# Optimization experiments

Hardware: AMD Instinct MI355X
Metric: run time of the kernel (lower is better)

Reference implementation:

```python
import jax, jax.numpy as jnp
import numpy as np

N_NODES = 100000
N_EDGES = 3200000
N_GRAPHS = 64
DIMS = [512, 1024, 512, 256, 128, 64, 32]
N_CLASSES = 10


def setup_inputs() -> dict:
    key = jax.random.key(0)
    ks = jax.random.split(key, 20)
    inp = {}
    inp['h'] = jax.random.normal(ks[0], (N_NODES, DIMS[0]), dtype=jnp.float32)
    inp['src'] = jax.random.randint(ks[1], (N_EDGES,), 0, N_NODES, dtype=jnp.int32)
    inp['dst'] = jax.random.randint(ks[2], (N_EDGES,), 0, N_NODES, dtype=jnp.int32)
    inp['graph_ids'] = jnp.sort(jax.random.randint(ks[3], (N_NODES,), 0, N_GRAPHS, dtype=jnp.int32))
    # GraphConv weights (glorot-like) and biases for the 6 layers
    for i in range(6):
        fi, fo = DIMS[i], DIMS[i + 1]
        scale = jnp.sqrt(2.0 / (fi + fo)).astype(jnp.float32)
        inp[f'W{i+1}'] = jax.random.normal(ks[4 + i], (fi, fo), dtype=jnp.float32) * scale
        inp[f'b{i+1}'] = jnp.zeros((fo,), dtype=jnp.float32)
    inp['Wc'] = jax.random.normal(ks[12], (DIMS[-1], N_CLASSES), dtype=jnp.float32) * 0.1
    inp['bc'] = jnp.zeros((N_CLASSES,), dtype=jnp.float32)
    return inp


def _graph_conv(h, W, b, src, dst, out_inv_sqrt, in_inv_sqrt):
    """DGL GraphConv, norm='both': D_dst^{-1/2} A (D_src^{-1/2} h) W + b.
    Apply W first when it shrinks the feature dim (DGL's mult-first trick)."""
    fi, fo = W.shape
    if fi > fo:
        h = h @ W  # shrink before aggregating
    h = h * out_inv_sqrt[:, None]
    agg = jax.ops.segment_sum(h[src], dst, num_segments=N_NODES)  # SpMM
    agg = agg * in_inv_sqrt[:, None]
    if fi <= fo:
        agg = agg @ W
    return agg + b


def reference(h, src, dst, graph_ids, W1, b1, W2, b2, W3, b3, W4, b4, W5, b5, W6, b6, Wc, bc):
    ones_e = jnp.ones((N_EDGES,), dtype=jnp.float32)
    out_deg = jax.ops.segment_sum(ones_e, src, num_segments=N_NODES)
    in_deg = jax.ops.segment_sum(ones_e, dst, num_segments=N_NODES)
    out_inv_sqrt = jax.lax.rsqrt(jnp.clip(out_deg, 1.0))  # allow_zero_in_degree -> clamp
    in_inv_sqrt = jax.lax.rsqrt(jnp.clip(in_deg, 1.0))
    for (W, b) in [(W1, b1), (W2, b2), (W3, b3), (W4, b4), (W5, b5), (W6, b6)]:
        h = jax.nn.relu(_graph_conv(h, W, b, src, dst, out_inv_sqrt, in_inv_sqrt))
    # dgl.mean_nodes over batched graph
    sums = jax.ops.segment_sum(h, graph_ids, num_segments=N_GRAPHS)
    counts = jax.ops.segment_sum(jnp.ones((N_NODES,), jnp.float32), graph_ids, num_segments=N_GRAPHS)
    hg = sums / jnp.clip(counts, 1.0)[:, None]
    return hg @ Wc + bc  # [N_GRAPHS, n_classes]
```

## Files before the change

### kernel.cpp

```cpp
#include <hip/hip_runtime.h>

#define N_NODES 100000
#define N_EDGES 3200000
#define N_GRAPHS 64
#define M_PAD   100096
#define CAP     128

typedef unsigned short u16;
typedef __bf16 bf16x8 __attribute__((ext_vector_type(8)));
typedef float f32x4 __attribute__((ext_vector_type(4)));
typedef unsigned int u32x4 __attribute__((ext_vector_type(4)));
typedef __attribute__((address_space(3))) unsigned int lds_u32;
typedef __attribute__((address_space(1))) unsigned int glb_u32;

__device__ inline u16 f2bf(float f) {
  unsigned u = __float_as_uint(f);
  unsigned r = (u + 0x7fffu + ((u >> 16) & 1u)) >> 16;
  return (u16)r;
}
__device__ inline float bf2f(u16 h) {
  return __uint_as_float(((unsigned)h) << 16);
}

#define E4 (N_EDGES / 4)
__global__ void k_build(const int* __restrict__ src, const int* __restrict__ dst,
                        int* __restrict__ odeg, int* __restrict__ cur,
                        int* __restrict__ colp) {
  int t = blockIdx.x * blockDim.x + threadIdx.x;
  if (t >= E4) return;
  int s[4], d[4], pos[4];
  #pragma unroll
  for (int q = 0; q < 4; ++q) {
    int e = t + q * E4;
    s[q] = src[e];
    d[q] = dst[e];
  }
  #pragma unroll
  for (int q = 0; q < 4; ++q) atomicAdd(&odeg[s[q]], 1);
  #pragma unroll
  for (int q = 0; q < 4; ++q) pos[q] = atomicAdd(&cur[d[q]], 1);
  #pragma unroll
  for (int q = 0; q < 4; ++q)
    if (pos[q] < CAP)
      __builtin_nontemporal_store(s[q], &colp[(size_t)d[q] * CAP + pos[q]]);
}

__global__ void k_rsqrt(const int* __restrict__ odeg, const int* __restrict__ ideg,
                        float* __restrict__ a, float* __restrict__ bI) {
  int v = blockIdx.x * blockDim.x + threadIdx.x;
  if (v < N_NODES) {
    a[v]  = rsqrtf(fmaxf((float)odeg[v], 1.0f));
    bI[v] = rsqrtf(fmaxf((float)ideg[v], 1.0f));
  }
}

__global__ void k_prep(const float* __restrict__ x, const float* __restrict__ ascl,
                       u16* __restrict__ y) {
  int i = blockIdx.x * blockDim.x + threadIdx.x;
  if (i >= N_NODES * 128) return;
  int row = i >> 7;
  float s = ascl[row];
  float4 v = ((const float4*)x)[i];
  uint2 o;
  o.x = (unsigned)f2bf(v.x * s) | ((unsigned)f2bf(v.y * s) << 16);
  o.y = (unsigned)f2bf(v.z * s) | ((unsigned)f2bf(v.w * s) << 16);
  ((uint2*)y)[i] = o;
}

__global__ void k_wt(const float* __restrict__ W, u16* __restrict__ Wt, int fi, int fo) {
  int idx = blockIdx.x * blockDim.x + threadIdx.x;
  if (idx >= fi * fo) return;
  int n = idx / fi, k = idx % fi;
  Wt[idx] = f2bf(W[(size_t)k * fo + n]);
}

template<int BM, int BN, int WM, int WN>
__global__ __launch_bounds__(256) void k_mfma(
    const u16* __restrict__ A, const u16* __restrict__ Wt,
    const float* __restrict__ bias, const float* __restrict__ rowscale,
    u16* __restrict__ C, int N, int K, int flags)
{
  constexpr int BK = 32;
  constexpr int WX = BN / WN;
  constexpr int WY = BM / WM;
  static_assert(WX * WY == 4, "4 waves");
  constexpr int TM = WM / 16;
  constexpr int TN = WN / 16;
  constexpr int CA = BM / 16;
  constexpr int CB = BN / 16;

  __shared__ __align__(1024) u16 As[BM * BK];
  __shared__ __align__(1024) u16 Bs[BN * BK];

  const int G   = gridDim.x;
  const int lin = blockIdx.x;
  const int xcd = lin & 7, pp = lin >> 3;
  const int q8  = G >> 3,  r8 = G & 7;
  const int nbid = (xcd < r8 ? xcd * (q8 + 1) : r8 * (q8 + 1) + (xcd - r8) * q8) + pp;
  const int gx = N / BN;
  const int bm = (nbid / gx) * BM;
  const int bn = (nbid % gx) * BN;

  const int tid  = threadIdx.x;
  const int wave = tid >> 6;
  const int lane = tid & 63;
  const int wx = wave % WX;
  const int wy = wave / WX;

  const int lm = lane & 15;
  const int lc = lane >> 4;

  const int srA = (lane >> 2);
  const int spA = lane & 3;
  f32x4 acc[TM][TN] = {};

  for (int k0 = 0; k0 < K; k0 += BK) {
    #pragma unroll
    for (int q0 = 0; q0 < CA; q0 += 4) {
      int q = q0 + wave;
      if (q < CA) {
        int rl = q * 16 + srA;
        int c  = (spA - (rl >> 1)) & 3;
        const u16* g = A + (size_t)(bm + rl) * K + k0 + c * 8;
        __builtin_amdgcn_global_load_lds((const glb_u32*)g, (lds_u32*)(As + q * 512), 16, 0, 0);
      }
    }
    #pragma unroll
    for (int q0 = 0; q0 < CB; q0 += 4) {
      int q = q0 + wave;
      if (q < CB) {
        int rl = q * 16 + srA;
        int c  = (spA - (rl >> 1)) & 3;
        const u16* g = Wt + (size_t)(bn + rl) * K + k0 + c * 8;
        __builtin_amdgcn_global_load_lds((const glb_u32*)g, (lds_u32*)(Bs + q * 512), 16, 0, 0);
      }
    }
    __syncthreads();

    bf16x8 af[TM], bfr[TN];
    #pragma unroll
    for (int i = 0; i < TM; ++i) {
      int rl = wy * WM + i * 16 + lm;
      int p = (lc + (rl >> 1)) & 3;
      af[i] = *(const bf16x8*)(As + rl * 32 + p * 8);
    }
    #pragma unroll
    for (int j = 0; j < TN; ++j) {
      int rl = wx * WN + j * 16 + lm;
      int p = (lc + (rl >> 1)) & 3;
      bfr[j] = *(const bf16x8*)(Bs + rl * 32 + p * 8);
    }
    #pragma unroll
    for (int i = 0; i < TM; ++i)
      #pragma unroll
      for (int j = 0; j < TN; ++j)
        acc[i][j] = __builtin_amdgcn_mfma_f32_16x16x32_bf16(af[i], bfr[j], acc[i][j], 0, 0, 0);
    __syncthreads();
  }

  const bool do_br = flags & 1;
  const bool do_rs = flags & 2;
  #pragma unroll
  for (int i = 0; i < TM; ++i) {
    #pragma unroll
    for (int j = 0; j < TN; ++j) {
      int col = bn + wx * WN + j * 16 + lm;
      float bv = do_br ? bias[col] : 0.f;
      #pragma unroll
      for (int r = 0; r < 4; ++r) {
        int row = bm + wy * WM + i * 16 + lc * 4 + r;
        float v = acc[i][j][r];
        if (do_rs) v *= rowscale[row];
        if (do_br) v = fmaxf(v + bv, 0.f);
        C[(size_t)row * N + col] = f2bf(v);
      }
    }
  }
}

template<int D>
__global__ __launch_bounds__(256) void k_spmm(
    const int* __restrict__ deg, const int* __restrict__ colp,
    const u16* __restrict__ X, const float* __restrict__ dscale,
    const float* __restrict__ bias, u16* __restrict__ Y, int relu_bias)
{
  constexpr int TPR = D / 8;
  constexpr int EPW = 64 / TPR;
  const int lane = threadIdx.x & 63;
  const int node = blockIdx.x * 4 + (threadIdx.x >> 6);
  const int g = lane / TPR;
  const int c = (lane % TPR) * 8;
  const int* cl = colp + (size_t)node * CAP;
  int e = deg[node];
  e = e < CAP ? e : CAP;
  float acc[8] = {};
  int j = 0;
  for (; j + 4 * EPW <= e; j += 4 * EPW) {
    int u0 = cl[j + g];
    int u1 = cl[j + g + EPW];
    int u2 = cl[j + g + 2 * EPW];
    int u3 = cl[j + g + 3 * EPW];
    u32x4 v0 = *(const u32x4*)(X + (size_t)u0 * D + c);
    u32x4 v1 = *(const u32x4*)(X + (size_t)u1 * D + c);
    u32x4 v2 = *(const u32x4*)(X + (size_t)u2 * D + c);
    u32x4 v3 = *(const u32x4*)(X + (size_t)u3 * D + c);
    #pragma unroll
    for (int q = 0; q < 4; ++q) {
      acc[2*q]   += __uint_as_float(v0[q] << 16);
      acc[2*q+1] += __uint_as_float(v0[q] & 0xffff0000u);
      acc[2*q]   += __uint_as_float(v1[q] << 16);
      acc[2*q+1] += __uint_as_float(v1[q] & 0xffff0000u);
      acc[2*q]   += __uint_as_float(v2[q] << 16);
      acc[2*q+1] += __uint_as_float(v2[q] & 0xffff0000u);
      acc[2*q]   += __uint_as_float(v3[q] << 16);
      acc[2*q+1] += __uint_as_float(v3[q] & 0xffff0000u);
    }
  }
  for (; j < e; j += EPW) {
    if (j + g < e) {
      int u = cl[j + g];
      u32x4 v = *(const u32x4*)(X + (size_t)u * D + c);
      #pragma unroll
      for (int q = 0; q < 4; ++q) {
        acc[2*q]   += __uint_as_float(v[q] << 16);
        acc[2*q+1] += __uint_as_float(v[q] & 0xffff0000u);
      }
    }
  }
  if constexpr (EPW > 1) {
    #pragma unroll
    for (int off = TPR; off < 64; off <<= 1) {
      #pragma unroll
      for (int q = 0; q < 8; ++q) acc[q] += __shfl_xor(acc[q], off);
    }
  }
  if (lane < TPR) {
    float dv = dscale[node];
    #pragma unroll
    for (int q = 0; q < 8; ++q) acc[q] *= dv;
    if (relu_bias) {
      #pragma unroll
      for (int q = 0; q < 8; ++q) acc[q] = fmaxf(acc[q] + bias[c + q], 0.f);
    }
    u32x4 o;
    o[0] = (unsigned)f2bf(acc[0]) | ((unsigned)f2bf(acc[1]) << 16);
    o[1] = (unsigned)f2bf(acc[2]) | ((unsigned)f2bf(acc[3]) << 16);
    o[2] = (unsigned)f2bf(acc[4]) | ((unsigned)f2bf(acc[5]) << 16);
    o[3] = (unsigned)f2bf(acc[6]) | ((unsigned)f2bf(acc[7]) << 16);
    __builtin_nontemporal_store(o, (u32x4*)(Y + (size_t)node * D + c));
  }
}

__global__ __launch_bounds__(256) void k_pool(const u16* __restrict__ h6,
                                              const int* __restrict__ gid,
                                              float* __restrict__ sums,
                                              float* __restrict__ cnts)
{
  __shared__ float acc[N_GRAPHS * 32];
  __shared__ float cnt[N_GRAPHS];
  int t = threadIdx.x;
  for (int k = t; k < N_GRAPHS * 32; k += 256) acc[k] = 0.f;
  if (t < N_GRAPHS) cnt[t] = 0.f;
  __syncthreads();
  int base = blockIdx.x * 256;
  int c = t & 31;
  int nl = t >> 5;
  for (int p = 0; p < 32; ++p) {
    int node = base + p * 8 + nl;
    if (node < N_NODES) {
      int g = gid[node];
      atomicAdd(&acc[g * 32 + c], bf2f(h6[(size_t)node * 32 + c]));
      if (c == 0) atomicAdd(&cnt[g], 1.0f);
    }
  }
  __syncthreads();
  for (int k = t; k < N_GRAPHS * 32; k += 256)
    if (acc[k] != 0.f) atomicAdd(&sums[k], acc[k]);
  if (t < N_GRAPHS && cnt[t] != 0.f) atomicAdd(&cnts[t], cnt[t]);
}

__global__ void k_final(const float* __restrict__ sums, const float* __restrict__ cnts,
                        const float* __restrict__ Wc, const float* __restrict__ bc,
                        float* __restrict__ out)
{
  int t = threadIdx.x;
  if (t >= N_GRAPHS * 10) return;
  int g = t / 10, cls = t % 10;
  float inv = 1.0f / fmaxf(cnts[g], 1.0f);
  float v = bc[cls];
  #pragma unroll
  for (int k = 0; k < 32; ++k)
    v += sums[g * 32 + k] * inv * Wc[k * 10 + cls];
  out[t] = v;
}

extern "C" void kernel_launch(void* const* d_in, const int* in_sizes, int n_in,
                              void* d_out, int out_size, void* d_ws, size_t ws_size,
                              hipStream_t stream)
{
  const float* h   = (const float*)d_in[0];
  const int*   src = (const int*)d_in[1];
  const int*   dst = (const int*)d_in[2];
  const int*   gid = (const int*)d_in[3];
  const float* W[6]; const float* b[6];
  for (int i = 0; i < 6; ++i) { W[i] = (const float*)d_in[4 + 2 * i]; b[i] = (const float*)d_in[5 + 2 * i]; }
  const float* Wc = (const float*)d_in[16];
  const float* bc = (const float*)d_in[17];
  float* out = (float*)d_out;

  const int FI[6] = {512, 1024, 512, 256, 128, 64};
  const int FO[6] = {1024, 512, 256, 128, 64, 32};

  char* p = (char*)d_ws;
  auto take = [&](size_t bytes) -> void* {
    void* r = (void*)p;
    p += (bytes + 255) & ~(size_t)255;
    return r;
  };
  u16* hb   = (u16*)take((size_t)M_PAD * 512 * 2);
  u16* bufA = (u16*)take((size_t)M_PAD * 512 * 2);
  u16* bufB = (u16*)take((size_t)M_PAD * 1024 * 2);
  u16* Wt[6];
  for (int i = 0; i < 6; ++i) Wt[i] = (u16*)take((size_t)FI[i] * FO[i] * 2);
  int*   colp = (int*)take((size_t)N_NODES * CAP * 4);
  int*   odeg = (int*)take((size_t)N_NODES * 4);
  int*   cur  = (int*)take((size_t)N_NODES * 4);
  float* ascl = (float*)take((size_t)M_PAD * 4);
  float* bscl = (float*)take((size_t)N_NODES * 4);
  float* psum = (float*)take((size_t)N_GRAPHS * 32 * 4);
  float* pcnt = (float*)take((size_t)N_GRAPHS * 4);
  if ((size_t)((char*)p - (char*)d_ws) > ws_size) return;

  hipMemsetAsync(odeg, 0, (size_t)N_NODES * 4 * 2 + 256, stream);
  hipMemsetAsync(psum, 0, (size_t)N_GRAPHS * 32 * 4, stream);
  hipMemsetAsync(pcnt, 0, (size_t)N_GRAPHS * 4, stream);

  k_build<<<(E4 + 255) / 256, 256, 0, stream>>>(src, dst, odeg, cur, colp);
  k_rsqrt<<<(N_NODES + 255) / 256, 256, 0, stream>>>(odeg, cur, ascl, bscl);

  k_prep<<<(N_NODES * 128 + 255) / 256, 256, 0, stream>>>(h, ascl, hb);
  for (int i = 0; i < 6; ++i)
    k_wt<<<(FI[i] * FO[i] + 255) / 256, 256, 0, stream>>>(W[i], Wt[i], FI[i], FO[i]);

  const int GY = M_PAD / 128;
  const int GS = N_NODES / 4;

  k_spmm<512><<<GS, 256, 0, stream>>>(cur, colp, hb, bscl, nullptr, bufA, 0);
  k_mfma<128,128,64,64><<<8 * GY, 256, 0, stream>>>(bufA, Wt[0], b[0], nullptr, bufB, 1024, 512, 1);

  k_mfma<128,128,64,64><<<4 * GY, 256, 0, stream>>>(bufB, Wt[1], nullptr, ascl, bufA, 512, 1024, 2);
  k_spmm<512><<<GS, 256, 0, stream>>>(cur, colp, bufA, bscl, b[1], hb, 1);

  k_mfma<128,128,64,64><<<2 * GY, 256, 0, stream>>>(hb, Wt[2], nullptr, ascl, bufA, 256, 512, 2);
  k_spmm<256><<<GS, 256, 0, stream>>>(cur, colp, bufA, bscl, b[2], hb, 1);

  k_mfma<128,128,64,64><<<1 * GY, 256, 0, stream>>>(hb, Wt[3], nullptr, ascl, bufA, 128, 256, 2);
  k_spmm<128><<<GS, 256, 0, stream>>>(cur, colp, bufA, bscl, b[3], hb, 1);

  k_mfma<128,64,64,32><<<1 * GY, 256, 0, stream>>>(hb, Wt[4], nullptr, ascl, bufA, 64, 128, 2);
  k_spmm<64><<<GS, 256, 0, stream>>>(cur, colp, bufA, bscl, b[4], hb, 1);

  k_mfma<128,32,64,16><<<1 * GY, 256, 0, stream>>>(hb, Wt[5], nullptr, ascl, bufA, 32, 64, 2);
  k_spmm<32><<<GS, 256, 0, stream>>>(cur, colp, bufA, bscl, b[5], hb, 1);

  k_pool<<<(N_NODES + 255) / 256, 256, 0, stream>>>(hb, gid, psum, pcnt);
  k_final<<<1, 640, 0, stream>>>(psum, pcnt, Wc, bc, out);
}
```

Before: 2.541 ms.

## Build CSR via two-pass bucketed scatter and merge rsqrt/weight-transpose kernels

The CSR build changes from per-destination global atomics with scattered writes into a two-pass bucket sort. Edges are first appended as packed (dst,src) pairs into 128-node buckets, then each bucket is placed using LDS atomics into the padded column array. The goal is less global atomic contention on cur and better locality for colp writes, at the cost of an extra pass over 3.2M 8-byte entries stored in bufB. The degree-rsqrt kernel and the six weight-transpose launches are also merged into one kernel to cut launch overhead.

```diff
diff --git a/kernel.cpp b/kernel.cpp
--- a/kernel.cpp
+++ b/kernel.cpp
@@ -5,8 +5,11 @@
 #define N_GRAPHS 64
 #define M_PAD   100096
 #define CAP     128
+#define NBKT    782
+#define BCAP    6144
 
 typedef unsigned short u16;
+typedef unsigned long long u64;
 typedef __bf16 bf16x8 __attribute__((ext_vector_type(8)));
 typedef float f32x4 __attribute__((ext_vector_type(4)));
 typedef unsigned int u32x4 __attribute__((ext_vector_type(4)));
@@ -23,9 +26,9 @@
 }
 
 #define E4 (N_EDGES / 4)
-__global__ void k_build(const int* __restrict__ src, const int* __restrict__ dst,
-                        int* __restrict__ odeg, int* __restrict__ cur,
-                        int* __restrict__ colp) {
+__global__ void k_scat(const int* __restrict__ src, const int* __restrict__ dst,
+                       int* __restrict__ odeg, int* __restrict__ bcnt,
+                       u64* __restrict__ btab) {
   int t = blockIdx.x * blockDim.x + threadIdx.x;
   if (t >= E4) return;
   int s[4], d[4], pos[4];
@@ -38,20 +41,76 @@
   #pragma unroll
   for (int q = 0; q < 4; ++q) atomicAdd(&odeg[s[q]], 1);
   #pragma unroll
-  for (int q = 0; q < 4; ++q) pos[q] = atomicAdd(&cur[d[q]], 1);
+  for (int q = 0; q < 4; ++q) pos[q] = atomicAdd(&bcnt[d[q] >> 7], 1);
   #pragma unroll
   for (int q = 0; q < 4; ++q)
-    if (pos[q] < CAP)
-      __builtin_nontemporal_store(s[q], &colp[(size_t)d[q] * CAP + pos[q]]);
-}
-
-__global__ void k_rsqrt(const int* __restrict__ odeg, const int* __restrict__ ideg,
-                        float* __restrict__ a, float* __restrict__ bI) {
-  int v = blockIdx.x * blockDim.x + threadIdx.x;
-  if (v < N_NODES) {
-    a[v]  = rsqrtf(fmaxf((float)odeg[v], 1.0f));
-    bI[v] = rsqrtf(fmaxf((float)ideg[v], 1.0f));
-  }
+    if (pos[q] < BCAP)
+      btab[(size_t)(d[q] >> 7) * BCAP + pos[q]] = ((u64)(unsigned)d[q] << 32) | (unsigned)s[q];
+}
+
+__global__ __launch_bounds__(256) void k_bkt(const int* __restrict__ bcnt,
+                                             const u64* __restrict__ btab,
+                                             int* __restrict__ colp,
+                                             int* __restrict__ cur) {
+  __shared__ int cnt[128];
+  const int b = blockIdx.x;
+  const int t = threadIdx.x;
+  if (t < 128) cnt[t] = 0;
+  __syncthreads();
+  int n = bcnt[b];
+  n = n < BCAP ? n : BCAP;
+  const u64* tb = btab + (size_t)b * BCAP;
+  for (int i = t; i < n; i += 256) {
+    u64 v = tb[i];
+    int d = (int)(v >> 32);
+    int s = (int)(v & 0xffffffffu);
+    int pos = atomicAdd(&cnt[d & 127], 1);
+    if (pos < CAP) colp[(size_t)d * CAP + pos] = s;
+  }
+  __syncthreads();
+  int node = b * 128 + t;
+  if (t < 128 && node < N_NODES) cur[node] = cnt[t];
+}
+
+struct WtArgs { const float* W[6]; u16* Wt[6]; };
+
+__global__ __launch_bounds__(256) void k_aux(const int* __restrict__ odeg,
+                                             const int* __restrict__ ideg,
+                                             float* __restrict__ a,
+                                             float* __restrict__ bI,
+                                             WtArgs wa) {
+  int blk = blockIdx.x;
+  if (blk < 391) {
+    int v = blk * 256 + threadIdx.x;
+    if (v < N_NODES) {
+      a[v]  = rsqrtf(fmaxf((float)odeg[v], 1.0f));
+      bI[v] = rsqrtf(fmaxf((float)ideg[v], 1.0f));
+    }
+    return;
+  }
+  int r = blk - 391;
+  #define WT_LAYER(i, FIc, FOc)                                        \
+    {                                                                  \
+      int idx = r * 256 + (int)threadIdx.x;                            \
+      constexpr int fi = FIc, fo = FOc;                                \
+      if (idx < fi * fo) {                                             \
+        int n = idx / fi, k = idx % fi;                                \
+        wa.Wt[i][idx] = f2bf(wa.W[i][(size_t)k * fo + n]);             \
+      }                                                                \
+      return;                                                          \
+    }
+  if (r < 2048) WT_LAYER(0, 512, 1024)
+  r -= 2048;
+  if (r < 2048) WT_LAYER(1, 1024, 512)
+  r -= 2048;
+  if (r < 512)  WT_LAYER(2, 512, 256)
+  r -= 512;
+  if (r < 128)  WT_LAYER(3, 256, 128)
+  r -= 128;
+  if (r < 32)   WT_LAYER(4, 128, 64)
+  r -= 32;
+  WT_LAYER(5, 64, 32)
+  #undef WT_LAYER
 }
 
 __global__ void k_prep(const float* __restrict__ x, const float* __restrict__ ascl,
@@ -65,13 +124,6 @@
   o.x = (unsigned)f2bf(v.x * s) | ((unsigned)f2bf(v.y * s) << 16);
   o.y = (unsigned)f2bf(v.z * s) | ((unsigned)f2bf(v.w * s) << 16);
   ((uint2*)y)[i] = o;
-}
-
-__global__ void k_wt(const float* __restrict__ W, u16* __restrict__ Wt, int fi, int fo) {
-  int idx = blockIdx.x * blockDim.x + threadIdx.x;
-  if (idx >= fi * fo) return;
-  int n = idx / fi, k = idx % fi;
-  Wt[idx] = f2bf(W[(size_t)k * fo + n]);
 }
 
 template<int BM, int BN, int WM, int WN>
@@ -324,6 +376,7 @@
   for (int i = 0; i < 6; ++i) Wt[i] = (u16*)take((size_t)FI[i] * FO[i] * 2);
   int*   colp = (int*)take((size_t)N_NODES * CAP * 4);
   int*   odeg = (int*)take((size_t)N_NODES * 4);
+  int*   bcnt = (int*)take((size_t)NBKT * 4);
   int*   cur  = (int*)take((size_t)N_NODES * 4);
   float* ascl = (float*)take((size_t)M_PAD * 4);
   float* bscl = (float*)take((size_t)N_NODES * 4);
@@ -331,16 +384,19 @@
   float* pcnt = (float*)take((size_t)N_GRAPHS * 4);
   if ((size_t)((char*)p - (char*)d_ws) > ws_size) return;
 
-  hipMemsetAsync(odeg, 0, (size_t)N_NODES * 4 * 2 + 256, stream);
+  u64* btab = (u64*)bufB;
+
+  hipMemsetAsync(odeg, 0, (size_t)((char*)cur - (char*)odeg), stream);
   hipMemsetAsync(psum, 0, (size_t)N_GRAPHS * 32 * 4, stream);
   hipMemsetAsync(pcnt, 0, (size_t)N_GRAPHS * 4, stream);
 
-  k_build<<<(E4 + 255) / 256, 256, 0, stream>>>(src, dst, odeg, cur, colp);
-  k_rsqrt<<<(N_NODES + 255) / 256, 256, 0, stream>>>(odeg, cur, ascl, bscl);
-
+  k_scat<<<(E4 + 255) / 256, 256, 0, stream>>>(src, dst, odeg, bcnt, btab);
+  k_bkt<<<NBKT, 256, 0, stream>>>(bcnt, btab, colp, cur);
+
+  WtArgs wa;
+  for (int i = 0; i < 6; ++i) { wa.W[i] = W[i]; wa.Wt[i] = Wt[i]; }
+  k_aux<<<391 + 4776, 256, 0, stream>>>(odeg, cur, ascl, bscl, wa);
   k_prep<<<(N_NODES * 128 + 255) / 256, 256, 0, stream>>>(h, ascl, hb);
-  for (int i = 0; i < 6; ++i)
-    k_wt<<<(FI[i] * FO[i] + 255) / 256, 256, 0, stream>>>(W[i], Wt[i], FI[i], FO[i]);
 
   const int GY = M_PAD / 128;
   const int GS = N_NODES / 4;
```

Result: slower. 3.129 ms (+23.2%).
